# Optimization experiments

Measured on AMD Instinct MI355X. Metric: run time of the kernel, lower is better.

Reference implementation:

```python
import jax, jax.numpy as jnp
import numpy as np

B, N, E, DIN, DOUT = 8, 4096, 160, 15, 15


def _mha(q, k, v, in_w, in_b, out_w, out_b, h):
    # torch.nn.MultiheadAttention math: packed in_proj, per-head scaled dot attn, out_proj.
    e = q.shape[-1]
    d = e // h
    scale = 1.0 / np.sqrt(d)

    def proj(x, w, b):
        y = x @ w.T + b
        return jnp.moveaxis(y.reshape(y.shape[:-1] + (h, d)), -2, -3)  # [..., h, L, d]

    qh = proj(q, in_w[:e], in_b[:e])
    kh = proj(k, in_w[e:2 * e], in_b[e:2 * e])
    vh = proj(v, in_w[2 * e:], in_b[2 * e:])
    a = jax.nn.softmax(jnp.einsum('...hld,...hmd->...hlm', qh, kh) * scale, axis=-1)
    o = jnp.einsum('...hlm,...hmd->...hld', a, vh)
    o = jnp.moveaxis(o, -3, -2).reshape(q.shape)
    return o @ out_w.T + out_b


def _attn_layer(seq, Wq, Wk, Wv, in_w, in_b, out_w, out_b, h):
    # AttentionLayer: extra Wq/Wk/Wv projections feeding the MHA
    return _mha(seq @ Wq, seq @ Wk, seq @ Wv, in_w, in_b, out_w, out_b, h)


def setup_inputs():
    key = jax.random.key(0)
    ks = jax.random.split(key, 20)
    s = 1.0 / np.sqrt(E)
    p = lambda i, shape: jax.random.normal(ks[i], shape, dtype=jnp.float32) * s
    return {
        'X_batch': jax.random.normal(ks[0], (B, N, E), dtype=jnp.float32),
        'in_idx': jax.random.randint(ks[1], (B, N, DIN), 0, N),
        'out_idx': jax.random.randint(ks[2], (B, N, DOUT), 0, N),
        'iWq': p(3, (E, E)), 'iWk': p(4, (E, E)), 'iWv': p(5, (E, E)),
        'i_in_w': p(6, (3 * E, E)), 'i_in_b': jnp.zeros(3 * E, jnp.float32),
        'i_out_w': p(7, (E, E)), 'i_out_b': jnp.zeros(E, jnp.float32),
        'oWq': p(8, (E, E)), 'oWk': p(9, (E, E)), 'oWv': p(10, (E, E)),
        'o_in_w': p(11, (3 * E, E)), 'o_in_b': jnp.zeros(3 * E, jnp.float32),
        'o_out_w': p(12, (E, E)), 'o_out_b': jnp.zeros(E, jnp.float32),
        'f_in_w': p(13, (3 * E, E)), 'f_in_b': jnp.zeros(3 * E, jnp.float32),
        'f_out_w': p(14, (E, E)), 'f_out_b': jnp.zeros(E, jnp.float32),
        'lin_w': p(15, (E, E)), 'lin_b': jnp.zeros(E, jnp.float32),
    }


def reference(X_batch, in_idx, out_idx,
              iWq, iWk, iWv, i_in_w, i_in_b, i_out_w, i_out_b,
              oWq, oWk, oWv, o_in_w, o_in_b, o_out_w, o_out_b,
              f_in_w, f_in_b, f_out_w, f_out_b, lin_w, lin_b):
    b_ix = jnp.arange(X_batch.shape[0])[:, None, None]
    self_f = X_batch[:, :, None, :]                                   # [B,N,1,E]
    seq_in = jnp.concatenate([self_f, X_batch[b_ix, in_idx]], axis=2)  # [B,N,1+DIN,E]
    seq_out = jnp.concatenate([self_f, X_batch[b_ix, out_idx]], axis=2)
    a_in = _attn_layer(seq_in, iWq, iWk, iWv, i_in_w, i_in_b, i_out_w, i_out_b, 5)
    a_out = _attn_layer(seq_out, oWq, oWk, oWv, o_in_w, o_in_b, o_out_w, o_out_b, 5)
    a = jnp.concatenate([a_in, a_out], axis=2)                         # [B,N,2+DIN+DOUT,E]
    f = _mha(a, a, a, f_in_w, f_in_b, f_out_w, f_out_b, 1)
    pooled = jnp.max(f, axis=2)                                        # max over sequence dim
    return jax.nn.elu(pooled @ lin_w.T + lin_b)
```

## Files before the change

### kernel.cpp

```cpp
#include <hip/hip_runtime.h>
#include <hip/hip_bf16.h>
#include <math.h>

#define NTH 256

typedef __bf16 bf16x8 __attribute__((ext_vector_type(8)));
typedef float  f32x4  __attribute__((ext_vector_type(4)));
typedef unsigned short ushort;
typedef ushort u16x8 __attribute__((ext_vector_type(8)));

__device__ __forceinline__ ushort f2bf(float x){
    union { float f; unsigned int u; } v; v.f = x;
    unsigned int r = v.u + 0x7fffu + ((v.u >> 16) & 1u);
    return (ushort)(r >> 16);
}
__device__ __forceinline__ float bf2f(ushort h){
    union { unsigned int u; float f; } v; v.u = ((unsigned int)h) << 16;
    return v.f;
}

__global__ void prep_combined_bf(const float* __restrict__ Wq, const float* __restrict__ Wk,
                                 const float* __restrict__ Wv, const float* __restrict__ in_w,
                                 ushort* __restrict__ dh)
{
    int o = blockIdx.x*NTH + threadIdx.x;
    if (o >= 76800) return;
    int c = o/160, j = o - c*160;
    const float* Wsel = (c<160) ? Wq : (c<320) ? Wk : Wv;
    const float* wrow = Wsel + j*160;
    const float* irow = in_w + c*160;
    float s = 0.f;
    for (int k=0;k<160;k++) s = fmaf(wrow[k], irow[k], s);
    dh[o] = f2bf(s);
}

__global__ void prep_H_split(const float* __restrict__ f_in_w, const float* __restrict__ out_w,
                             ushort* __restrict__ dh, float* __restrict__ tmp)
{
    int o = blockIdx.x*NTH + threadIdx.x;
    if (o >= 76800) return;
    int n = o/160, k = o - n*160;
    float s = 0.f;
    for (int c=0;c<160;c++) s = fmaf(f_in_w[n*160+c], out_w[c*160+k], s);
    if (n < 320) dh[o] = f2bf(s);
    else         tmp[(n-320)*160 + k] = s;
}

__global__ void prep_H_fold(const float* __restrict__ fo, const float* __restrict__ Hv,
                            ushort* __restrict__ dh)
{
    int o = blockIdx.x*NTH + threadIdx.x;
    if (o >= 25600) return;
    int n = o/160, k = o - n*160;
    float s = 0.f;
    for (int j=0;j<160;j++) s = fmaf(fo[n*160+j], Hv[j*160+k], s);
    dh[(320+n)*160 + k] = f2bf(s);
}

__global__ void prep_cvec(const float* __restrict__ f_in_w, const float* __restrict__ out_b,
                          const float* __restrict__ f_in_b, float* __restrict__ cvt)
{
    int n = blockIdx.x*NTH + threadIdx.x;
    if (n >= 480) return;
    float s = f_in_b[n];
    for (int c=0;c<160;c++) s = fmaf(f_in_w[n*160+c], out_b[c], s);
    cvt[n] = s;
}

__global__ void prep_cvec_fold(const float* __restrict__ fo, const float* __restrict__ cvt,
                               float* __restrict__ cv)
{
    int n = blockIdx.x*NTH + threadIdx.x;
    if (n >= 480) return;
    if (n < 320){ cv[n] = cvt[n]; return; }
    int m = n - 320;
    float s = 0.f;
    for (int j=0;j<160;j++) s = fmaf(fo[m*160+j], cvt[320+j], s);
    cv[n] = s;
}

__global__ void prep_conv_bf1(const float* __restrict__ src, ushort* __restrict__ dh, int n)
{
    int o = blockIdx.x*NTH + threadIdx.x;
    if (o >= n) return;
    dh[o] = f2bf(src[o]);
}

__global__ void prep_conv_bf2(const float* __restrict__ src,
                              ushort* __restrict__ dh, ushort* __restrict__ dl, int n)
{
    int o = blockIdx.x*NTH + threadIdx.x;
    if (o >= n) return;
    float s = src[o];
    ushort h = f2bf(s);
    dh[o] = h; dl[o] = f2bf(s - bf2f(h));
}

__global__ __launch_bounds__(NTH)
void gemm_mfma_lin(const float* __restrict__ A,
                   const ushort* __restrict__ Wh, const ushort* __restrict__ Wl,
                   const float* __restrict__ bias, float* __restrict__ C, int N)
{
    __shared__ ushort sAh[128*40], sAl[128*40];
    __shared__ ushort sWh[160*40], sWl[160*40];

    const int tid = threadIdx.x;
    const int lane = tid & 63, wave = tid >> 6;
    const int wm = wave >> 1, wn = wave & 1;
    const int ln = lane & 15, g = lane >> 4;
    const long m0 = (long)blockIdx.x * 128;
    const int  n0 = blockIdx.y * 160;

    f32x4 acc[4][5];
#pragma unroll
    for (int mt=0;mt<4;mt++)
#pragma unroll
        for (int nt=0;nt<5;nt++)
#pragma unroll
            for (int r=0;r<4;r++) acc[mt][nt][r] = 0.f;

    for (int k0=0;k0<160;k0+=32){
#pragma unroll
        for (int i=0;i<4;i++){
            int f = tid + 256*i;
            int m = f >> 3, seg = f & 7;
            float4 v = *(const float4*)(A + (m0+m)*160 + k0 + seg*4);
            ushort4 hv, lv;
            hv.x = f2bf(v.x); lv.x = f2bf(v.x - bf2f(hv.x));
            hv.y = f2bf(v.y); lv.y = f2bf(v.y - bf2f(hv.y));
            hv.z = f2bf(v.z); lv.z = f2bf(v.z - bf2f(hv.z));
            hv.w = f2bf(v.w); lv.w = f2bf(v.w - bf2f(hv.w));
            *(ushort4*)(sAh + m*40 + seg*4) = hv;
            *(ushort4*)(sAl + m*40 + seg*4) = lv;
        }
#pragma unroll
        for (int i=0;i<5;i++){
            int e = tid + 256*i;
            int pl = (e >= 640);
            int idx = pl ? e-640 : e;
            int n = idx >> 2, seg = idx & 3;
            const ushort* src = (pl ? Wl : Wh) + (long)(n0+n)*160 + k0 + seg*8;
            ushort* dst = (pl ? sWl : sWh) + n*40 + seg*8;
            *(uint4*)dst = *(const uint4*)src;
        }
        __syncthreads();

        bf16x8 ah[4], al[4];
#pragma unroll
        for (int mt=0;mt<4;mt++){
            int off = (wm*64 + mt*16 + ln)*40 + g*8;
            ah[mt] = *(const bf16x8*)(sAh + off);
            al[mt] = *(const bf16x8*)(sAl + off);
        }
#pragma unroll
        for (int nt=0;nt<5;nt++){
            int offw = (wn*80 + nt*16 + ln)*40 + g*8;
            bf16x8 bh = *(const bf16x8*)(sWh + offw);
            bf16x8 bl = *(const bf16x8*)(sWl + offw);
#pragma unroll
            for (int mt=0;mt<4;mt++){
                acc[mt][nt] = __builtin_amdgcn_mfma_f32_16x16x32_bf16(ah[mt], bh, acc[mt][nt], 0,0,0);
                acc[mt][nt] = __builtin_amdgcn_mfma_f32_16x16x32_bf16(al[mt], bh, acc[mt][nt], 0,0,0);
                acc[mt][nt] = __builtin_amdgcn_mfma_f32_16x16x32_bf16(ah[mt], bl, acc[mt][nt], 0,0,0);
            }
        }
        __syncthreads();
    }

#pragma unroll
    for (int nt=0;nt<5;nt++){
        int col = n0 + wn*80 + nt*16 + ln;
        float bv = bias[col];
#pragma unroll
        for (int mt=0;mt<4;mt++){
#pragma unroll
            for (int r=0;r<4;r++){
                long row = m0 + wm*64 + mt*16 + g*4 + r;
                float x = acc[mt][nt][r] + bv;
                x = x > 0.f ? x : expm1f(x);
                C[row*N + col] = x;
            }
        }
    }
}

__global__ __launch_bounds__(NTH)
void gemm_bf(const ushort* __restrict__ A0, const ushort* __restrict__ A1,
             const ushort* __restrict__ Wh0, const ushort* __restrict__ Wh1,
             const float* __restrict__ b0, const float* __restrict__ b1,
             ushort* __restrict__ C0, ushort* __restrict__ C1, int N)
{
    const int z = blockIdx.z;
    const ushort* A  = z ? A1 : A0;
    const ushort* Wh = z ? Wh1 : Wh0;
    const float* bias = z ? b1 : b0;
    ushort* C = z ? C1 : C0;

    __shared__ ushort sA[128*40];
    __shared__ ushort sW[160*40];

    const int tid = threadIdx.x;
    const int lane = tid & 63, wave = tid >> 6;
    const int wm = wave >> 1, wn = wave & 1;
    const int ln = lane & 15, g = lane >> 4;
    const long m0 = (long)blockIdx.x * 128;
    const int  n0 = blockIdx.y * 160;

    f32x4 acc[4][5];
#pragma unroll
    for (int mt=0;mt<4;mt++)
#pragma unroll
        for (int nt=0;nt<5;nt++)
#pragma unroll
            for (int r=0;r<4;r++) acc[mt][nt][r] = 0.f;

    for (int k0=0;k0<160;k0+=32){
#pragma unroll
        for (int i=0;i<2;i++){
            int e = tid + 256*i;
            int m = e >> 2, seg = e & 3;
            *(uint4*)(sA + m*40 + seg*8) =
                *(const uint4*)(A + (m0+m)*160 + k0 + seg*8);
        }
#pragma unroll
        for (int i=0;i<3;i++){
            int e = tid + 256*i;
            if (e < 640){
                int n = e >> 2, seg = e & 3;
                *(uint4*)(sW + n*40 + seg*8) =
                    *(const uint4*)(Wh + (long)(n0+n)*160 + k0 + seg*8);
            }
        }
        __syncthreads();

        bf16x8 af[4];
#pragma unroll
        for (int mt=0;mt<4;mt++)
            af[mt] = *(const bf16x8*)(sA + (wm*64 + mt*16 + ln)*40 + g*8);
#pragma unroll
        for (int nt=0;nt<5;nt++){
            bf16x8 bh = *(const bf16x8*)(sW + (wn*80 + nt*16 + ln)*40 + g*8);
#pragma unroll
            for (int mt=0;mt<4;mt++)
                acc[mt][nt] = __builtin_amdgcn_mfma_f32_16x16x32_bf16(af[mt], bh, acc[mt][nt], 0,0,0);
        }
        __syncthreads();
    }

#pragma unroll
    for (int nt=0;nt<5;nt++){
        int col = n0 + wn*80 + nt*16 + ln;
        float bv = bias[col];
#pragma unroll
        for (int mt=0;mt<4;mt++){
#pragma unroll
            for (int r=0;r<4;r++){
                long row = m0 + wm*64 + mt*16 + g*4 + r;
                C[row*N + col] = f2bf(acc[mt][nt][r] + bv);
            }
        }
    }
}

__global__ __launch_bounds__(64)
void attn_layer_mfma(const ushort* __restrict__ XPi, const ushort* __restrict__ XPo,
                     const int* __restrict__ in_idx, const int* __restrict__ out_idx,
                     ushort* __restrict__ Oi, ushort* __restrict__ Oo, int node_base)
{
    const ushort* XP = blockIdx.y ? XPo : XPi;
    const int*  idx  = blockIdx.y ? out_idx : in_idx;
    ushort* O        = blockIdx.y ? Oo : Oi;

    __shared__ ushort XPg[16*496];
    __shared__ ushort Pall[5*16*24];

    const int lane = threadIdx.x;
    const int ln = lane & 15, q = lane >> 4;
    const int node = node_base + blockIdx.x;
    const int bb = node >> 12, nn = node & 4095;

    int idxv = nn;
    if (lane >= 1 && lane < 16) idxv = idx[(long)node*15 + lane-1];

#pragma unroll
    for (int i=0;i<15;i++){
        int e = lane + 64*i;
        int r = e/60, c = e - r*60;
        int rowg = __shfl(idxv, r);
        *(uint4*)(XPg + r*496 + c*8) =
            *(const uint4*)(XP + (long)(bb*4096 + rowg)*480 + c*8);
    }
    __syncthreads();

    const float scale = 0.17677669529663687f;
#pragma unroll
    for (int h=0;h<5;h++){
        bf16x8 ka = *(const bf16x8*)(XPg + ln*496 + 160 + h*32 + q*8);
        bf16x8 qb = *(const bf16x8*)(XPg + ln*496 +       h*32 + q*8);
        f32x4 s = {0.f,0.f,0.f,0.f};
        s = __builtin_amdgcn_mfma_f32_16x16x32_bf16(ka, qb, s, 0,0,0);
        float x[4], m = -1e30f;
#pragma unroll
        for (int r=0;r<4;r++){ x[r] = s[r]*scale; m = fmaxf(m, x[r]); }
        m = fmaxf(m, __shfl_xor(m, 16));
        m = fmaxf(m, __shfl_xor(m, 32));
        float e0[4], sum = 0.f;
#pragma unroll
        for (int r=0;r<4;r++){ e0[r] = __expf(x[r]-m); sum += e0[r]; }
        sum += __shfl_xor(sum, 16);
        sum += __shfl_xor(sum, 32);
        float inv = 1.f/sum;
        ushort4 pw;
        pw.x = f2bf(e0[0]*inv); pw.y = f2bf(e0[1]*inv);
        pw.z = f2bf(e0[2]*inv); pw.w = f2bf(e0[3]*inv);
        *(ushort4*)(Pall + h*384 + ln*24 + q*4) = pw;
    }
    __syncthreads();

#pragma unroll
    for (int h=0;h<5;h++){
        u16x8 ta;
#pragma unroll
        for (int jj=0;jj<8;jj++) ta[jj] = 0;
        if (q < 2) ta = *(const u16x8*)(Pall + h*384 + ln*24 + q*8);
        bf16x8 ap = *(bf16x8*)&ta;
#pragma unroll
        for (int half=0; half<2; half++){
            u16x8 tb;
#pragma unroll
            for (int jj=0;jj<8;jj++) tb[jj] = 0;
            if (q < 2){
#pragma unroll
                for (int jj=0;jj<8;jj++)
                    tb[jj] = XPg[(q*8+jj)*496 + 320 + h*32 + half*16 + ln];
            }
            bf16x8 bv = *(bf16x8*)&tb;
            f32x4 o = {0.f,0.f,0.f,0.f};
            o = __builtin_amdgcn_mfma_f32_16x16x32_bf16(ap, bv, o, 0,0,0);
#pragma unroll
            for (int r=0;r<4;r++)
                O[(long)(blockIdx.x*16 + q*4 + r)*160 + h*32 + half*16 + ln] = f2bf(o[r]);
        }
    }
}

__global__ __launch_bounds__(NTH)
void fused_fq_attn_pool(const ushort* __restrict__ O_i, const ushort* __restrict__ O_o,
                        const ushort* __restrict__ Hi, const ushort* __restrict__ Ho,
                        const float* __restrict__ c_i, const float* __restrict__ c_o,
                        const float* __restrict__ fb, float* __restrict__ pooled,
                        int node_base)
{
    __shared__ ushort sFQ[4*32*328];
    __shared__ ushort sVt[4*160*40];
    __shared__ ushort sP [4*32*40];

    const int tid  = threadIdx.x;
    const int lane = tid & 63, wave = tid >> 6;
    const int ln = lane & 15, g = lane >> 4;
    const int wl = wave >> 1, wn = wave & 1;
    const int nl0 = blockIdx.x * 4;

    const ushort* Ow = wl ? O_o : O_i;
    const ushort* Hw = wl ? Ho  : Hi;
    const float*  cw = wl ? c_o : c_i;

    bf16x8 ofr[4][5];
#pragma unroll
    for (int nd=0; nd<4; nd++)
#pragma unroll
        for (int kc=0; kc<5; kc++)
            ofr[nd][kc] = *(const bf16x8*)(Ow + ((long)(nl0+nd)*16 + ln)*160 + kc*32 + g*8);

    bf16x8 hf[5], hn[5];
#pragma unroll
    for (int kc=0; kc<5; kc++)
        hf[kc] = *(const bf16x8*)(Hw + (long)(wn*16 + ln)*160 + kc*32 + g*8);

    for (int t=0; t<15; t++){
        const int n0 = t*32;
        if (t < 14){
            const ushort* hrow = Hw + (long)((t+1)*32 + wn*16 + ln)*160;
#pragma unroll
            for (int kc=0; kc<5; kc++)
                hn[kc] = *(const bf16x8*)(hrow + kc*32 + g*8);
        }

        f32x4 acc[4];
#pragma unroll
        for (int nd=0; nd<4; nd++)
#pragma unroll
            for (int r=0;r<4;r++) acc[nd][r] = 0.f;

#pragma unroll
        for (int kc=0; kc<5; kc++)
#pragma unroll
            for (int nd=0; nd<4; nd++)
                acc[nd] = __builtin_amdgcn_mfma_f32_16x16x32_bf16(hf[kc], ofr[nd][kc], acc[nd], 0,0,0);

        const int cb0 = n0 + wn*16 + g*4;
        float4 cb = *(const float4*)(cw + cb0);
        if (n0 < 320){
#pragma unroll
            for (int nd=0; nd<4; nd++){
                ushort4 w4;
                w4.x = f2bf(acc[nd][0] + cb.x);
                w4.y = f2bf(acc[nd][1] + cb.y);
                w4.z = f2bf(acc[nd][2] + cb.z);
                w4.w = f2bf(acc[nd][3] + cb.w);
                *(ushort4*)(sFQ + nd*10496 + (wl*16 + ln)*328 + cb0) = w4;
            }
        } else {
            const int c0 = cb0 - 320;
#pragma unroll
            for (int nd=0; nd<4; nd++){
                sVt[nd*6400 + (c0+0)*40 + wl*16 + ln] = f2bf(acc[nd][0] + cb.x);
                sVt[nd*6400 + (c0+1)*40 + wl*16 + ln] = f2bf(acc[nd][1] + cb.y);
                sVt[nd*6400 + (c0+2)*40 + wl*16 + ln] = f2bf(acc[nd][2] + cb.z);
                sVt[nd*6400 + (c0+3)*40 + wl*16 + ln] = f2bf(acc[nd][3] + cb.w);
            }
        }
#pragma unroll
        for (int kc=0; kc<5; kc++) hf[kc] = hn[kc];
    }
    __syncthreads();

    const ushort* myQ = sFQ + wave*10496;
    const ushort* myV = sVt + wave*6400;
    ushort*       myP = sP  + wave*1280;

    f32x4 sc[2][2];
#pragma unroll
    for (int ti=0; ti<2; ti++)
#pragma unroll
        for (int tj=0; tj<2; tj++){
            f32x4 a = {0.f,0.f,0.f,0.f};
#pragma unroll
            for (int kc=0; kc<5; kc++){
                bf16x8 ka = *(const bf16x8*)(myQ + (tj*16+ln)*328 + 160 + kc*32 + g*8);
                bf16x8 qb = *(const bf16x8*)(myQ + (ti*16+ln)*328 +       kc*32 + g*8);
                a = __builtin_amdgcn_mfma_f32_16x16x32_bf16(ka, qb, a, 0,0,0);
            }
            sc[ti][tj] = a;
        }

    const float scale = 0.07905694150420949f;
#pragma unroll
    for (int ti=0; ti<2; ti++){
        float x[2][4], m = -1e30f;
#pragma unroll
        for (int tj=0; tj<2; tj++)
#pragma unroll
            for (int r=0;r<4;r++){ x[tj][r] = sc[ti][tj][r]*scale; m = fmaxf(m, x[tj][r]); }
        m = fmaxf(m, __shfl_xor(m, 16));
        m = fmaxf(m, __shfl_xor(m, 32));
        float sum = 0.f;
#pragma unroll
        for (int tj=0; tj<2; tj++)
#pragma unroll
            for (int r=0;r<4;r++){ x[tj][r] = __expf(x[tj][r]-m); sum += x[tj][r]; }
        sum += __shfl_xor(sum, 16);
        sum += __shfl_xor(sum, 32);
        float inv = 1.f/sum;
#pragma unroll
        for (int tj=0; tj<2; tj++){
            ushort4 pw;
            pw.x = f2bf(x[tj][0]*inv); pw.y = f2bf(x[tj][1]*inv);
            pw.z = f2bf(x[tj][2]*inv); pw.w = f2bf(x[tj][3]*inv);
            *(ushort4*)(myP + (ti*16+ln)*40 + tj*16 + g*4) = pw;
        }
    }
    __syncthreads();

    bf16x8 ap[2];
#pragma unroll
    for (int mi=0; mi<2; mi++)
        ap[mi] = *(const bf16x8*)(myP + (mi*16+ln)*40 + g*8);

    const long node = (long)node_base + nl0 + wave;
#pragma unroll
    for (int nt=0; nt<10; nt++){
        bf16x8 bv = *(const bf16x8*)(myV + (nt*16+ln)*40 + g*8);
        float vmax = -1e30f;
#pragma unroll
        for (int mi=0; mi<2; mi++){
            f32x4 o = {0.f,0.f,0.f,0.f};
            o = __builtin_amdgcn_mfma_f32_16x16x32_bf16(ap[mi], bv, o, 0,0,0);
#pragma unroll
            for (int r=0;r<4;r++) vmax = fmaxf(vmax, o[r]);
        }
        vmax = fmaxf(vmax, __shfl_xor(vmax, 16));
        vmax = fmaxf(vmax, __shfl_xor(vmax, 32));
        if (g == 0){
            int col = nt*16 + ln;
            pooled[node*160 + col] = vmax + fb[col];
        }
    }
}

extern "C" void kernel_launch(void* const* d_in, const int* in_sizes, int n_in,
                              void* d_out, int out_size, void* d_ws, size_t ws_size,
                              hipStream_t stream)
{
    const float* X       = (const float*)d_in[0];
    const int*   in_idx  = (const int*)  d_in[1];
    const int*   out_idx = (const int*)  d_in[2];
    const float* iWq     = (const float*)d_in[3];
    const float* iWk     = (const float*)d_in[4];
    const float* iWv     = (const float*)d_in[5];
    const float* i_in_w  = (const float*)d_in[6];
    const float* i_in_b  = (const float*)d_in[7];
    const float* i_out_w = (const float*)d_in[8];
    const float* i_out_b = (const float*)d_in[9];
    const float* oWq     = (const float*)d_in[10];
    const float* oWk     = (const float*)d_in[11];
    const float* oWv     = (const float*)d_in[12];
    const float* o_in_w  = (const float*)d_in[13];
    const float* o_in_b  = (const float*)d_in[14];
    const float* o_out_w = (const float*)d_in[15];
    const float* o_out_b = (const float*)d_in[16];
    const float* f_in_w  = (const float*)d_in[17];
    const float* f_in_b  = (const float*)d_in[18];
    const float* f_out_w = (const float*)d_in[19];
    const float* f_out_b = (const float*)d_in[20];
    const float* lin_w   = (const float*)d_in[21];
    const float* lin_b   = (const float*)d_in[22];

    float* ws = (float*)d_ws;
    float* pooled = ws;
    float* c_i    = pooled + 5242880;
    float* c_o    = c_i + 480;
    float* cvt_i  = c_o + 480;
    float* cvt_o  = cvt_i + 480;
    float* Hvt_i  = cvt_o + 480;
    float* Hvt_o  = Hvt_i + 25600;
    ushort* ub    = (ushort*)(Hvt_o + 25600);
    ushort* Xb    = ub;
    ushort* XPb_i = Xb + 5242880;
    ushort* XPb_o = XPb_i + 15728640;
    ushort* Wci_h = XPb_o + 15728640;
    ushort* Wco_h = Wci_h + 76800;
    ushort* Hi_h  = Wco_h + 76800;
    ushort* Ho_h  = Hi_h  + 76800;
    ushort* li_h  = Ho_h  + 76800;
    ushort* li_l  = li_h  + 25600;
    ushort* sb_us = li_l + 25600;
    const unsigned long long fixed = 23825280ULL;

    size_t avail = ws_size / 4;
    int ns = 32768;
    while (ns > 64 && fixed + 2560ULL*ns > avail) ns >>= 1;

    ushort* O_i = sb_us;
    ushort* O_o = O_i + (size_t)2560*ns;

    prep_combined_bf<<<300,NTH,0,stream>>>(iWq,iWk,iWv,i_in_w, Wci_h);
    prep_combined_bf<<<300,NTH,0,stream>>>(oWq,oWk,oWv,o_in_w, Wco_h);
    prep_H_split<<<300,NTH,0,stream>>>(f_in_w, i_out_w, Hi_h, Hvt_i);
    prep_H_split<<<300,NTH,0,stream>>>(f_in_w, o_out_w, Ho_h, Hvt_o);
    prep_H_fold<<<100,NTH,0,stream>>>(f_out_w, Hvt_i, Hi_h);
    prep_H_fold<<<100,NTH,0,stream>>>(f_out_w, Hvt_o, Ho_h);
    prep_cvec<<<2,NTH,0,stream>>>(f_in_w, i_out_b, f_in_b, cvt_i);
    prep_cvec<<<2,NTH,0,stream>>>(f_in_w, o_out_b, f_in_b, cvt_o);
    prep_cvec_fold<<<2,NTH,0,stream>>>(f_out_w, cvt_i, c_i);
    prep_cvec_fold<<<2,NTH,0,stream>>>(f_out_w, cvt_o, c_o);
    prep_conv_bf2<<<100,NTH,0,stream>>>(lin_w, li_h, li_l, 25600);
    prep_conv_bf1<<<20480,NTH,0,stream>>>(X, Xb, 5242880);

    dim3 g1(256, 3, 2);
    gemm_bf<<<g1,NTH,0,stream>>>(Xb, Xb, Wci_h, Wco_h, i_in_b, o_in_b,
                                 XPb_i, XPb_o, 480);

    int S = 32768 / ns;
    for (int s=0;s<S;s++){
        int base = s*ns;
        dim3 ga(ns, 2);
        attn_layer_mfma<<<ga,64,0,stream>>>(XPb_i, XPb_o, in_idx, out_idx, O_i, O_o, base);
        fused_fq_attn_pool<<<ns/4,NTH,0,stream>>>(O_i, O_o, Hi_h, Ho_h, c_i, c_o,
                                                  f_out_b, pooled, base);
    }

    dim3 g6(256, 1);
    gemm_mfma_lin<<<g6,NTH,0,stream>>>(pooled, li_h, li_l, lin_b, (float*)d_out, 160);
}
```

Measured before the change: 879.8 us.

## Double waves per block in fused final-attention pooling kernel

Launches the fused FQ-attention-pool kernel with 512 threads instead of 256 and re-splits the work across eight waves. In the projection phase each wave now handles every fourth 16-column group instead of every second. In the attention phase each node is shared by two waves, each taking one query half and half of the output tiles. This halves the serial per-wave work, aiming for more latency hiding. The cost is larger blocks with the same shared memory footprint, which may lower the number of resident blocks, plus some redundant loads.

```diff
diff --git a/kernel.cpp b/kernel.cpp
--- a/kernel.cpp
+++ b/kernel.cpp
@@ -344,7 +344,7 @@
     }
 }
 
-__global__ __launch_bounds__(NTH)
+__global__ __launch_bounds__(512)
 void fused_fq_attn_pool(const ushort* __restrict__ O_i, const ushort* __restrict__ O_o,
                         const ushort* __restrict__ Hi, const ushort* __restrict__ Ho,
                         const float* __restrict__ c_i, const float* __restrict__ c_o,
@@ -358,7 +358,7 @@
     const int tid  = threadIdx.x;
     const int lane = tid & 63, wave = tid >> 6;
     const int ln = lane & 15, g = lane >> 4;
-    const int wl = wave >> 1, wn = wave & 1;
+    const int wl = wave >> 2, wn = wave & 3;
     const int nl0 = blockIdx.x * 4;
 
     const ushort* Ow = wl ? O_o : O_i;
@@ -377,81 +377,82 @@
     for (int kc=0; kc<5; kc++)
         hf[kc] = *(const bf16x8*)(Hw + (long)(wn*16 + ln)*160 + kc*32 + g*8);
 
-    for (int t=0; t<15; t++){
-        const int n0 = t*32;
-        if (t < 14){
-            const ushort* hrow = Hw + (long)((t+1)*32 + wn*16 + ln)*160;
+    for (int t=0; t<8; t++){
+        const int cg  = t*4 + wn;
+        const int cgn = cg + 4;
+        if (t < 7 && cgn < 30){
+            const ushort* hrow = Hw + (long)(cgn*16 + ln)*160;
 #pragma unroll
             for (int kc=0; kc<5; kc++)
                 hn[kc] = *(const bf16x8*)(hrow + kc*32 + g*8);
         }
 
-        f32x4 acc[4];
-#pragma unroll
-        for (int nd=0; nd<4; nd++)
-#pragma unroll
-            for (int r=0;r<4;r++) acc[nd][r] = 0.f;
-
-#pragma unroll
-        for (int kc=0; kc<5; kc++)
+        if (cg < 30){
+            f32x4 acc[4];
 #pragma unroll
             for (int nd=0; nd<4; nd++)
-                acc[nd] = __builtin_amdgcn_mfma_f32_16x16x32_bf16(hf[kc], ofr[nd][kc], acc[nd], 0,0,0);
-
-        const int cb0 = n0 + wn*16 + g*4;
-        float4 cb = *(const float4*)(cw + cb0);
-        if (n0 < 320){
-#pragma unroll
-            for (int nd=0; nd<4; nd++){
-                ushort4 w4;
-                w4.x = f2bf(acc[nd][0] + cb.x);
-                w4.y = f2bf(acc[nd][1] + cb.y);
-                w4.z = f2bf(acc[nd][2] + cb.z);
-                w4.w = f2bf(acc[nd][3] + cb.w);
-                *(ushort4*)(sFQ + nd*10496 + (wl*16 + ln)*328 + cb0) = w4;
+#pragma unroll
+                for (int r=0;r<4;r++) acc[nd][r] = 0.f;
+
+#pragma unroll
+            for (int kc=0; kc<5; kc++)
+#pragma unroll
+                for (int nd=0; nd<4; nd++)
+                    acc[nd] = __builtin_amdgcn_mfma_f32_16x16x32_bf16(hf[kc], ofr[nd][kc], acc[nd], 0,0,0);
+
+            const int cb0 = cg*16 + g*4;
+            float4 cb = *(const float4*)(cw + cb0);
+            if (cg < 20){
+#pragma unroll
+                for (int nd=0; nd<4; nd++){
+                    ushort4 w4;
+                    w4.x = f2bf(acc[nd][0] + cb.x);
+                    w4.y = f2bf(acc[nd][1] + cb.y);
+                    w4.z = f2bf(acc[nd][2] + cb.z);
+                    w4.w = f2bf(acc[nd][3] + cb.w);
+                    *(ushort4*)(sFQ + nd*10496 + (wl*16 + ln)*328 + cb0) = w4;
+                }
+            } else {
+                const int c0 = cb0 - 320;
+#pragma unroll
+                for (int nd=0; nd<4; nd++){
+                    sVt[nd*6400 + (c0+0)*40 + wl*16 + ln] = f2bf(acc[nd][0] + cb.x);
+                    sVt[nd*6400 + (c0+1)*40 + wl*16 + ln] = f2bf(acc[nd][1] + cb.y);
+                    sVt[nd*6400 + (c0+2)*40 + wl*16 + ln] = f2bf(acc[nd][2] + cb.z);
+                    sVt[nd*6400 + (c0+3)*40 + wl*16 + ln] = f2bf(acc[nd][3] + cb.w);
+                }
             }
-        } else {
-            const int c0 = cb0 - 320;
-#pragma unroll
-            for (int nd=0; nd<4; nd++){
-                sVt[nd*6400 + (c0+0)*40 + wl*16 + ln] = f2bf(acc[nd][0] + cb.x);
-                sVt[nd*6400 + (c0+1)*40 + wl*16 + ln] = f2bf(acc[nd][1] + cb.y);
-                sVt[nd*6400 + (c0+2)*40 + wl*16 + ln] = f2bf(acc[nd][2] + cb.z);
-                sVt[nd*6400 + (c0+3)*40 + wl*16 + ln] = f2bf(acc[nd][3] + cb.w);
-            }
         }
 #pragma unroll
         for (int kc=0; kc<5; kc++) hf[kc] = hn[kc];
     }
     __syncthreads();
 
-    const ushort* myQ = sFQ + wave*10496;
-    const ushort* myV = sVt + wave*6400;
-    ushort*       myP = sP  + wave*1280;
-
-    f32x4 sc[2][2];
-#pragma unroll
-    for (int ti=0; ti<2; ti++)
-#pragma unroll
-        for (int tj=0; tj<2; tj++){
-            f32x4 a = {0.f,0.f,0.f,0.f};
-#pragma unroll
-            for (int kc=0; kc<5; kc++){
-                bf16x8 ka = *(const bf16x8*)(myQ + (tj*16+ln)*328 + 160 + kc*32 + g*8);
-                bf16x8 qb = *(const bf16x8*)(myQ + (ti*16+ln)*328 +       kc*32 + g*8);
-                a = __builtin_amdgcn_mfma_f32_16x16x32_bf16(ka, qb, a, 0,0,0);
-            }
-            sc[ti][tj] = a;
-        }
+    const int nd = wave >> 1, th = wave & 1;
+    const ushort* myQ = sFQ + nd*10496;
+    const ushort* myV = sVt + nd*6400;
+    ushort*       myP = sP  + nd*1280;
+
+    f32x4 sc[2];
+#pragma unroll
+    for (int tj=0; tj<2; tj++){
+        f32x4 a = {0.f,0.f,0.f,0.f};
+#pragma unroll
+        for (int kc=0; kc<5; kc++){
+            bf16x8 ka = *(const bf16x8*)(myQ + (tj*16+ln)*328 + 160 + kc*32 + g*8);
+            bf16x8 qb = *(const bf16x8*)(myQ + (th*16+ln)*328 +       kc*32 + g*8);
+            a = __builtin_amdgcn_mfma_f32_16x16x32_bf16(ka, qb, a, 0,0,0);
+        }
+        sc[tj] = a;
+    }
 
     const float scale = 0.07905694150420949f;
-#pragma unroll
-    for (int ti=0; ti<2; ti++){
+    {
         float x[2][4], m = -1e30f;
 #pragma unroll
         for (int tj=0; tj<2; tj++)
 #pragma unroll
-            for (int r=0;r<4;r++){ x[tj][r] = sc[ti][tj][r]*scale; m = fmaxf(m, x[tj][r]); }
+            for (int r=0;r<4;r++){ x[tj][r] = sc[tj][r]*scale; m = fmaxf(m, x[tj][r]); }
         m = fmaxf(m, __shfl_xor(m, 16));
         m = fmaxf(m, __shfl_xor(m, 32));
         float sum = 0.f;
@@ -467,7 +468,7 @@
             ushort4 pw;
             pw.x = f2bf(x[tj][0]*inv); pw.y = f2bf(x[tj][1]*inv);
             pw.z = f2bf(x[tj][2]*inv); pw.w = f2bf(x[tj][3]*inv);
-            *(ushort4*)(myP + (ti*16+ln)*40 + tj*16 + g*4) = pw;
+            *(ushort4*)(myP + (th*16+ln)*40 + tj*16 + g*4) = pw;
         }
     }
     __syncthreads();
@@ -477,9 +478,10 @@
     for (int mi=0; mi<2; mi++)
         ap[mi] = *(const bf16x8*)(myP + (mi*16+ln)*40 + g*8);
 
-    const long node = (long)node_base + nl0 + wave;
-#pragma unroll
-    for (int nt=0; nt<10; nt++){
+    const long node = (long)node_base + nl0 + nd;
+#pragma unroll
+    for (int nt5=0; nt5<5; nt5++){
+        const int nt = th*5 + nt5;
         bf16x8 bv = *(const bf16x8*)(myV + (nt*16+ln)*40 + g*8);
         float vmax = -1e30f;
 #pragma unroll
@@ -576,7 +578,7 @@
         int base = s*ns;
         dim3 ga(ns, 2);
         attn_layer_mfma<<<ga,64,0,stream>>>(XPb_i, XPb_o, in_idx, out_idx, O_i, O_o, base);
-        fused_fq_attn_pool<<<ns/4,NTH,0,stream>>>(O_i, O_o, Hi_h, Ho_h, c_i, c_o,
+        fused_fq_attn_pool<<<ns/4,512,0,stream>>>(O_i, O_o, Hi_h, Ho_h, c_i, c_o,
                                                   f_out_b, pooled, base);
     }
 
```

Result: faster. 764.6 us (-13.1%).
